# Kernel optimization log

Hardware: AMD Instinct MI355X
Metric: run time of the kernel (lower is better)

Reference implementation:

```python
import jax, jax.numpy as jnp
import numpy as np


def _temporal_gated_conv(x, W, b):
    """x: (B,T,N,C) -> (B,T-Kt+1,N,Co). W: (1,Kt,C,2*Co), b: (2*Co,).
    Matches torch Conv2d(in,2*out,(1,Kt)) over (B,C,N,T) followed by GLU."""
    xh = x.transpose(0, 2, 1, 3)  # (B,N,T,C) as NHWC, kernel (1,Kt) over (N,T)
    y = jax.lax.conv_general_dilated(
        xh, W, window_strides=(1, 1), padding='VALID',
        dimension_numbers=('NHWC', 'HWIO', 'NHWC')) + b  # (B,N,T',2Co)
    lhs, rhs = jnp.split(y, 2, axis=-1)
    y = lhs * jax.nn.sigmoid(rhs)
    return y.transpose(0, 2, 1, 3)  # (B,T',N,Co)


def _spatial_graph_conv(x, cheb, Theta):
    """x: (B,T,N,C), cheb: (K,N,N), Theta: (K,C,Co).
    Faithful to torch code: step_x is CUMULATIVELY multiplied by T_k."""
    K = cheb.shape[0]
    cur = x
    acc = jnp.zeros(x.shape[:3] + (Theta.shape[-1],), dtype=x.dtype)
    for k in range(K):  # K is small and structural
        cur = jnp.einsum('mn,btnc->btmc', cheb[k], cur)
        acc = acc + jnp.einsum('btnc,co->btno', cur, Theta[k])
    return jax.nn.relu(acc)


def setup_inputs() -> dict:
    key = jax.random.key(0)
    ks = jax.random.split(key, 7)
    B, T, N, C = 16, 64, 1024, 2
    Kt, Kc, temporal_dim, spatial_dim = 3, 3, 64, 16
    s = 0.05
    return {
        'x': jax.random.normal(ks[0], (B, T, N, C), jnp.float32),
        'cheb': jax.random.normal(ks[1], (Kc, N, N), jnp.float32) * (1.0 / np.sqrt(N)),
        'W1': jax.random.normal(ks[2], (1, Kt, C, 2 * temporal_dim), jnp.float32) * s,
        'b1': jax.random.normal(ks[3], (2 * temporal_dim,), jnp.float32) * s,
        'Theta': jax.random.normal(ks[4], (Kc, temporal_dim, spatial_dim), jnp.float32) * s,
        'W2': jax.random.normal(ks[5], (1, Kt, spatial_dim, 2 * temporal_dim), jnp.float32) * s,
        'b2': jax.random.normal(ks[6], (2 * temporal_dim,), jnp.float32) * s,
    }


def reference(x, cheb, W1, b1, Theta, W2, b2):
    h = _temporal_gated_conv(x, W1, b1)          # (B, T-Kt+1, N, temporal_dim)
    h = _spatial_graph_conv(h, cheb, Theta)      # (B, T-Kt+1, N, spatial_dim)
    out = _temporal_gated_conv(h, W2, b2)        # (B, T-2*(Kt-1), N, temporal_dim)
    return out
```

## Files before the change

### kernel.cpp

```cpp
#include <hip/hip_runtime.h>
#include <stdint.h>

typedef __attribute__((ext_vector_type(8))) short bf16x8;
typedef __attribute__((ext_vector_type(4))) float f32x4;

__device__ __forceinline__ unsigned short f2bf(float f) {
  union { float f; unsigned u; } v; v.f = f;
  unsigned r = v.u + 0x7FFFu + ((v.u >> 16) & 1u);
  return (unsigned short)(r >> 16);
}

__device__ __forceinline__ float sigm(float x) { return 1.0f / (1.0f + __expf(-x)); }

__device__ __forceinline__ void gload16(const void* g, void* l) {
  __builtin_amdgcn_global_load_lds((const __attribute__((address_space(1))) void*)g,
                                   (__attribute__((address_space(3))) void*)l, 16, 0, 0);
}

__device__ __forceinline__ void bar() {
  __builtin_amdgcn_sched_barrier(0);
  __builtin_amdgcn_s_barrier();
  __builtin_amdgcn_sched_barrier(0);
}

__global__ void k0t(const float* __restrict__ cheb, unsigned short* __restrict__ cb1,
                    unsigned short* __restrict__ cb2, unsigned short* __restrict__ Pbig,
                    unsigned short* __restrict__ t0, unsigned short* __restrict__ t1) {
  __shared__ unsigned short t[64][65];
  const int z = blockIdx.z;
  const int c = threadIdx.x & 63, r4 = threadIdx.x >> 6;
  const int r0 = blockIdx.y * 64, c0 = blockIdx.x * 64;
  const float* src = cheb + (size_t)z * 1048576;
#pragma unroll
  for (int r = 0; r < 64; r += 4) {
    const int rr = r0 + r + r4;
    const unsigned short h = f2bf(src[(size_t)rr * 1024 + c0 + c]);
    t[r + r4][c] = h;
    if (z == 0) Pbig[(size_t)rr * 3072 + c0 + c] = h;
    else if (z == 1) cb1[(size_t)rr * 1024 + c0 + c] = h;
    else cb2[(size_t)rr * 1024 + c0 + c] = h;
  }
  __syncthreads();
  if (z == 2) return;
  unsigned short* dst = z ? t1 : t0;
#pragma unroll
  for (int r = 0; r < 64; r += 4)
    dst[(size_t)(c0 + r + r4) * 1024 + r0 + c] = t[c][r + r4];
}

__global__ __launch_bounds__(256) void gemm_splitk(
    const unsigned short* __restrict__ A1, const unsigned short* __restrict__ B1,
    float* __restrict__ C1,
    const unsigned short* __restrict__ A2, const unsigned short* __restrict__ B2,
    float* __restrict__ C2) {
  __shared__ __align__(16) unsigned short sA[128 * 32];
  __shared__ __align__(16) unsigned short sB[128 * 32];
  const unsigned short* Ap = blockIdx.z ? A2 : A1;
  const unsigned short* Bp = blockIdx.z ? B2 : B1;
  float* Cp = blockIdx.z ? C2 : C1;
  const int mb = blockIdx.x & 7, nb = blockIdx.x >> 3, ks = blockIdx.y;
  const int tid = threadIdx.x;
  const int lane = tid & 63;
  const int w = tid >> 6;
  const int m0 = mb * 128, n0 = nb * 128;
  const int wm = (w >> 1) * 64, wn = (w & 1) * 64;
  const int lr = lane & 15, lg = lane >> 4;
  const f32x4 ZV = {0.f, 0.f, 0.f, 0.f};
  f32x4 acc[4][4];
#pragma unroll
  for (int f = 0; f < 4; ++f)
#pragma unroll
    for (int g = 0; g < 4; ++g) acc[f][g] = ZV;
  const int r2 = tid >> 2, kp = tid & 3;
  const size_t rowA0 = (size_t)(m0 + r2) * 1024;
  const size_t rowA1 = (size_t)(m0 + 64 + r2) * 1024;
  const size_t rowB0 = (size_t)(n0 + r2) * 1024;
  const size_t rowB1 = (size_t)(n0 + 64 + r2) * 1024;
  unsigned short* la = &sA[w * 512];
  unsigned short* lb = &sB[w * 512];
  const int kbase = ks * 256;
  for (int k0 = kbase; k0 < kbase + 256; k0 += 32) {
    const int kc = k0 + kp * 8;
    gload16(Ap + rowA0 + kc, la);
    gload16(Ap + rowA1 + kc, la + 2048);
    gload16(Bp + rowB0 + kc, lb);
    gload16(Bp + rowB1 + kc, lb + 2048);
    __syncthreads();
    bf16x8 av[4], bv[4];
#pragma unroll
    for (int f = 0; f < 4; ++f)
      av[f] = *(const bf16x8*)&sA[(wm + f * 16 + lr) * 32 + lg * 8];
#pragma unroll
    for (int g = 0; g < 4; ++g)
      bv[g] = *(const bf16x8*)&sB[(wn + g * 16 + lr) * 32 + lg * 8];
#pragma unroll
    for (int f = 0; f < 4; ++f)
#pragma unroll
      for (int g = 0; g < 4; ++g)
        acc[f][g] = __builtin_amdgcn_mfma_f32_16x16x32_bf16(av[f], bv[g], acc[f][g], 0, 0, 0);
    __syncthreads();
  }
  float* Cb = Cp + (size_t)ks * 1048576;
#pragma unroll
  for (int f = 0; f < 4; ++f) {
    const int m = m0 + wm + f * 16 + lg * 4;
#pragma unroll
    for (int g = 0; g < 4; ++g) {
      const int col = n0 + wn + g * 16 + lr;
#pragma unroll
      for (int i = 0; i < 4; ++i)
        Cb[(size_t)(m + i) * 1024 + col] = acc[f][g][i];
    }
  }
}

__global__ void reducep(const float* __restrict__ S1, unsigned short* __restrict__ D1, int ld1, int co1,
                        const float* __restrict__ S2, unsigned short* __restrict__ D2, int ld2, int co2) {
  const float* S = blockIdx.z ? S2 : S1;
  unsigned short* D = blockIdx.z ? D2 : D1;
  const int ld = blockIdx.z ? ld2 : ld1;
  const int co = blockIdx.z ? co2 : co1;
  const int e = (blockIdx.x * 256 + threadIdx.x) * 4;
  const float4 a = *(const float4*)&S[e];
  const float4 b = *(const float4*)&S[1048576 + e];
  const float4 c = *(const float4*)&S[2097152 + e];
  const float4 d = *(const float4*)&S[3145728 + e];
  const int row = e >> 10, col = e & 1023;
  ushort4 o;
  o.x = f2bf(a.x + b.x + c.x + d.x);
  o.y = f2bf(a.y + b.y + c.y + d.y);
  o.z = f2bf(a.z + b.z + c.z + d.z);
  o.w = f2bf(a.w + b.w + c.w + d.w);
  *(ushort4*)&D[(size_t)row * ld + co + col] = o;
}

__device__ __forceinline__ void dec_chunk(int s, int& row, int& c) {
  const int r3 = (((s >> 2) ^ (s >> 4)) & 1) | (((s >> 3) & 1) << 1) | (((s >> 4) & 1) << 2);
  const int u = s ^ r3;
  row = u >> 2;
  c = u & 3;
}

__global__ __launch_bounds__(512, 2) void gemm_big(
    const unsigned short* __restrict__ A, const unsigned short* __restrict__ Bt,
    unsigned short* __restrict__ C) {
  constexpr int K = 3072, NT = 96;
  __shared__ __align__(16) unsigned short lds[4 * 16384];
  const int tid = threadIdx.x;
  const int lane = tid & 63, w = tid >> 6;
  const int wr = w >> 2, wc = w & 3;
  const int lr = lane & 15, lg = lane >> 4;
  const int lin = blockIdx.x;
  const int v = (lin & 7) * 31 + (lin >> 3);
  const int mb = v & 3, nb = v >> 2;
  const int m0 = mb * 256, n0 = nb * 256;

  int r0_, c0_, r1_, c1_;
  dec_chunk((w * 2 + 0) * 64 + lane, r0_, c0_);
  dec_chunk((w * 2 + 1) * 64 + lane, r1_, c1_);
  const unsigned short* sA0 = A + (size_t)(m0 + r0_) * K + c0_ * 8;
  const unsigned short* sA1 = A + (size_t)(m0 + r1_) * K + c1_ * 8;
  const unsigned short* sB0 = Bt + (size_t)(n0 + r0_) * K + c0_ * 8;
  const unsigned short* sB1 = Bt + (size_t)(n0 + r1_) * K + c1_ * 8;
  const int ldsoff0 = (w * 2 + 0) * 512, ldsoff1 = (w * 2 + 1) * 512;

  f32x4 acc[8][4];
  const f32x4 ZV = {0.f, 0.f, 0.f, 0.f};
#pragma unroll
  for (int f = 0; f < 8; ++f)
#pragma unroll
    for (int g = 0; g < 4; ++g) acc[f][g] = ZV;

  const int aoff = (((wr * 128 + lr) * 64 + lg * 16) ^ ((lr & 7) << 4));
  const int boff = (((wc * 64 + lr) * 64 + lg * 16) ^ ((lr & 7) << 4));

  bf16x8 avA[8], bvA[4], avB[8], bvB[4];

#define STAGE(T)                                               \
  do {                                                         \
    unsigned short* ba_ = lds + ((T) & 3) * 16384;             \
    const int k0_ = (T) * 32;                                  \
    gload16(sA0 + k0_, ba_ + ldsoff0);                         \
    gload16(sA1 + k0_, ba_ + ldsoff1);                         \
    gload16(sB0 + k0_, ba_ + 8192 + ldsoff0);                  \
    gload16(sB1 + k0_, ba_ + 8192 + ldsoff1);                  \
  } while (0)

#define DSREAD(T, AN, BN)                                      \
  do {                                                         \
    const char* rb_ = (const char*)lds + ((T) & 3) * 32768;    \
    _Pragma("unroll") for (int f_ = 0; f_ < 8; ++f_)           \
      AN[f_] = *(const bf16x8*)(rb_ + aoff + f_ * 1024);       \
    _Pragma("unroll") for (int g_ = 0; g_ < 4; ++g_)           \
      BN[g_] = *(const bf16x8*)(rb_ + 16384 + boff + g_ * 1024); \
  } while (0)

#define MFMAC(AC, BC)                                          \
  do {                                                         \
    __builtin_amdgcn_s_setprio(1);                             \
    _Pragma("unroll") for (int f_ = 0; f_ < 8; ++f_)           \
      _Pragma("unroll") for (int g_ = 0; g_ < 4; ++g_)         \
        acc[f_][g_] = __builtin_amdgcn_mfma_f32_16x16x32_bf16(AC[f_], BC[g_], acc[f_][g_], 0, 0, 0); \
    __builtin_amdgcn_s_setprio(0);                             \
  } while (0)

  STAGE(0); STAGE(1); STAGE(2); STAGE(3);
  asm volatile("s_waitcnt vmcnt(8)" ::: "memory");
  bar();
  DSREAD(0, avA, bvA);

  for (int tt = 0; tt < NT - 4; tt += 2) {
    DSREAD(tt + 1, avB, bvB);
    STAGE(tt + 4);
    MFMAC(avA, bvA);
    asm volatile("s_waitcnt vmcnt(8) lgkmcnt(0)" ::: "memory");
    bar();
    DSREAD(tt + 2, avA, bvA);
    STAGE(tt + 5);
    MFMAC(avB, bvB);
    asm volatile("s_waitcnt vmcnt(8) lgkmcnt(0)" ::: "memory");
    bar();
  }
  DSREAD(93, avB, bvB);
  MFMAC(avA, bvA);
  asm volatile("s_waitcnt vmcnt(4) lgkmcnt(0)" ::: "memory");
  bar();
  DSREAD(94, avA, bvA);
  MFMAC(avB, bvB);
  asm volatile("s_waitcnt vmcnt(0) lgkmcnt(0)" ::: "memory");
  bar();
  DSREAD(95, avB, bvB);
  MFMAC(avA, bvA);
  asm volatile("s_waitcnt lgkmcnt(0)" ::: "memory");
  __builtin_amdgcn_sched_barrier(0);
  MFMAC(avB, bvB);
#undef STAGE
#undef DSREAD
#undef MFMAC

#pragma unroll
  for (int g = 0; g < 4; ++g) {
    const int n = n0 + wc * 64 + g * 16;
    const size_t jb = (size_t)(n >> 4) * 16384;
#pragma unroll
    for (int f = 0; f < 8; ++f) {
      const int m = m0 + wr * 128 + f * 16 + lg * 4;
#pragma unroll
      for (int i = 0; i < 4; ++i)
        C[jb + (size_t)(m + i) * 16 + lr] = f2bf(fmaxf(acc[f][g][i], 0.f));
    }
  }
}

__global__ __launch_bounds__(256) void k1_fused(
    const float* __restrict__ x, const float* __restrict__ W1, const float* __restrict__ b1,
    const float* __restrict__ Theta, unsigned short* __restrict__ Zt) {
  __shared__ __align__(16) unsigned short hs[4 * 64 * 68];
  __shared__ __align__(16) unsigned short th[3 * 16 * 72];
  __shared__ __align__(16) unsigned short tr[64 * 68];
  const int tid = threadIdx.x, lane = tid & 63, w = tid >> 6;
  const int n0 = blockIdx.x * 64;
  const int bt0 = blockIdx.y * 4;
  const int bt = bt0 + w;
  const int b = bt / 62, t = bt - b * 62;
  float xv[6];
#pragma unroll
  for (int kt = 0; kt < 3; ++kt) {
    const float2 p = *(const float2*)&x[(size_t)((b * 64 + t + kt) * 1024 + n0 + lane) * 2];
    xv[kt * 2] = p.x;
    xv[kt * 2 + 1] = p.y;
  }
  float h[64];
#pragma unroll
  for (int ch = 0; ch < 64; ++ch) {
    float l = b1[ch], r = b1[64 + ch];
#pragma unroll
    for (int q = 0; q < 6; ++q) {
      l += xv[q] * W1[q * 128 + ch];
      r += xv[q] * W1[q * 128 + 64 + ch];
    }
    h[ch] = l * sigm(r);
  }
#pragma unroll
  for (int c8 = 0; c8 < 8; ++c8) {
    union { unsigned short u[8]; uint4 v; } pk;
#pragma unroll
    for (int j = 0; j < 8; ++j) pk.u[j] = f2bf(h[c8 * 8 + j]);
    *(uint4*)&hs[(w * 64 + lane) * 68 + c8 * 8] = pk.v;
  }
  for (int idx = tid; idx < 3072; idx += 256) {
    const int kc = idx >> 10, o = (idx >> 6) & 15, c = idx & 63;
    th[kc * 1152 + o * 72 + c] = f2bf(Theta[((kc << 6) | c) * 16 + o]);
  }
  __syncthreads();
  const int lr = lane & 15, lg = lane >> 4;
  const f32x4 ZV = {0.f, 0.f, 0.f, 0.f};
  for (int kc = 0; kc < 3; ++kc) {
    const bf16x8 av0 = *(const bf16x8*)&th[kc * 1152 + lr * 72 + lg * 8];
    const bf16x8 av1 = *(const bf16x8*)&th[kc * 1152 + lr * 72 + 32 + lg * 8];
    f32x4 acc[4];
#pragma unroll
    for (int ns = 0; ns < 4; ++ns) acc[ns] = ZV;
#pragma unroll
    for (int ns = 0; ns < 4; ++ns) {
      const bf16x8 bv0 = *(const bf16x8*)&hs[(w * 64 + ns * 16 + lr) * 68 + lg * 8];
      const bf16x8 bv1 = *(const bf16x8*)&hs[(w * 64 + ns * 16 + lr) * 68 + 32 + lg * 8];
      acc[ns] = __builtin_amdgcn_mfma_f32_16x16x32_bf16(av0, bv0, acc[ns], 0, 0, 0);
      acc[ns] = __builtin_amdgcn_mfma_f32_16x16x32_bf16(av1, bv1, acc[ns], 0, 0, 0);
    }
    if (kc) __syncthreads();
#pragma unroll
    for (int ns = 0; ns < 4; ++ns)
#pragma unroll
      for (int i = 0; i < 4; ++i)
        tr[(w * 16 + lg * 4 + i) * 68 + ns * 16 + lr] = f2bf(acc[ns][i]);
    __syncthreads();
#pragma unroll
    for (int rd = 0; rd < 2; ++rd) {
      const int cidx = rd * 256 + tid;
      const int rl = cidx >> 3, ck = cidx & 7;
      const uint4 v = *(const uint4*)&tr[rl * 68 + ck * 8];
      *(uint4*)&Zt[(size_t)(bt0 * 16 + rl) * 3072 + kc * 1024 + n0 + ck * 8] = v;
    }
  }
}

__global__ __launch_bounds__(256) void k3_out(
    const unsigned short* __restrict__ accb, const float* __restrict__ W2,
    const float* __restrict__ b2, float* __restrict__ out) {
  __shared__ __align__(16) unsigned short sW[128 * 72];
  const int tid = threadIdx.x, lane = tid & 63, w = tid >> 6;
  const int lr = lane & 15, lg = lane >> 4;
  const int n0 = blockIdx.x * 256;
  const int btp = blockIdx.y;
  const int b = btp / 60, tt = btp - b * 60;
  for (int idx = tid; idx < 2048; idx += 256) {
    const int ch = idx >> 4, k = 48 + (idx & 15);
    sW[ch * 72 + k] = 0;
  }
  for (int idx = tid; idx < 6144; idx += 256) {
    const int k = idx >> 7, ch = idx & 127;
    sW[ch * 72 + k] = f2bf(W2[idx]);
  }
  const int rowb = n0 + w * 64;
  const bf16x8 ZB = {0, 0, 0, 0, 0, 0, 0, 0};
  bf16x8 av[4][2];
#pragma unroll
  for (int f = 0; f < 4; ++f)
#pragma unroll
    for (int hh = 0; hh < 2; ++hh) {
      const int gk = hh * 32 + lg * 8;
      const int kt = gk >> 4, ci = gk & 15;
      av[f][hh] = ZB;
      if (kt < 3)
        av[f][hh] = *(const bf16x8*)&accb[(size_t)(b * 62 + tt + kt) * 16384 +
                                          (size_t)(rowb + f * 16 + lr) * 16 + ci];
    }
  __syncthreads();
  const size_t obase = (size_t)(b * 60 + tt) * 65536;
  const f32x4 ZV = {0.f, 0.f, 0.f, 0.f};
#pragma unroll
  for (int gl = 0; gl < 4; ++gl) {
    const int chl = gl * 16 + lr;
    const bf16x8 bl0 = *(const bf16x8*)&sW[chl * 72 + lg * 8];
    const bf16x8 bl1 = *(const bf16x8*)&sW[chl * 72 + 32 + lg * 8];
    const bf16x8 br0 = *(const bf16x8*)&sW[(64 + chl) * 72 + lg * 8];
    const bf16x8 br1 = *(const bf16x8*)&sW[(64 + chl) * 72 + 32 + lg * 8];
    f32x4 aL[4], aR[4];
#pragma unroll
    for (int f = 0; f < 4; ++f) { aL[f] = ZV; aR[f] = ZV; }
#pragma unroll
    for (int f = 0; f < 4; ++f) {
      aL[f] = __builtin_amdgcn_mfma_f32_16x16x32_bf16(av[f][0], bl0, aL[f], 0, 0, 0);
      aL[f] = __builtin_amdgcn_mfma_f32_16x16x32_bf16(av[f][1], bl1, aL[f], 0, 0, 0);
      aR[f] = __builtin_amdgcn_mfma_f32_16x16x32_bf16(av[f][0], br0, aR[f], 0, 0, 0);
      aR[f] = __builtin_amdgcn_mfma_f32_16x16x32_bf16(av[f][1], br1, aR[f], 0, 0, 0);
    }
    const float bbl = b2[chl], bbr = b2[64 + chl];
#pragma unroll
    for (int f = 0; f < 4; ++f)
#pragma unroll
      for (int i = 0; i < 4; ++i) {
        const float pl = aL[f][i] + bbl;
        const float pr = aR[f][i] + bbr;
        out[obase + (size_t)(rowb + f * 16 + lg * 4 + i) * 64 + chl] = pl * sigm(pr);
      }
  }
}

extern "C" void kernel_launch(void* const* d_in, const int* in_sizes, int n_in,
                              void* d_out, int out_size, void* d_ws, size_t ws_size,
                              hipStream_t stream) {
  const float* x    = (const float*)d_in[0];
  const float* cheb = (const float*)d_in[1];
  const float* W1   = (const float*)d_in[2];
  const float* b1   = (const float*)d_in[3];
  const float* Th   = (const float*)d_in[4];
  const float* W2   = (const float*)d_in[5];
  const float* b2   = (const float*)d_in[6];
  float* out = (float*)d_out;

  char* ws = (char*)d_ws;
  const size_t MB = 1u << 20;
  unsigned short* cb1  = (unsigned short*)(ws);
  unsigned short* cb2  = (unsigned short*)(ws + 2 * MB);
  unsigned short* Pbig = (unsigned short*)(ws + 4 * MB);
  unsigned short* t0   = (unsigned short*)(ws + 10 * MB);
  unsigned short* t1   = (unsigned short*)(ws + 12 * MB);
  unsigned short* Qb   = (unsigned short*)(ws + 14 * MB);
  unsigned short* accb = (unsigned short*)(ws + 14 * MB);
  float*          P1f  = (float*)(ws + 48 * MB);
  float*          Qf   = (float*)(ws + 64 * MB);
  float*          P2f  = (float*)(ws + 80 * MB);
  unsigned short* Zt   = (unsigned short*)d_out;

  k0t<<<dim3(16, 16, 3), 256, 0, stream>>>(cheb, cb1, cb2, Pbig, t0, t1);
  gemm_splitk<<<dim3(64, 4, 2), 256, 0, stream>>>(cb1, t0, P1f, cb2, t1, Qf);
  reducep<<<dim3(1024, 1, 2), 256, 0, stream>>>(P1f, Pbig, 3072, 1024, Qf, Qb, 1024, 0);
  gemm_splitk<<<dim3(64, 4, 1), 256, 0, stream>>>(Qb, t0, P2f, Qb, t0, P2f);
  reducep<<<dim3(1024, 1, 1), 256, 0, stream>>>(P2f, Pbig, 3072, 2048, P2f, Pbig, 3072, 2048);
  k1_fused<<<dim3(16, 248), 256, 0, stream>>>(x, W1, b1, Th, Zt);
  gemm_big<<<dim3(248), dim3(512), 0, stream>>>(Pbig, Zt, accb);
  k3_out<<<dim3(4, 960), 256, 0, stream>>>(accb, W2, b2, out);
}
```

Before: 286.0 us.

## Restructure big GEMM main loop into split-phase ping-pong schedule with half-tile reads

Replaces the double-register-buffered main loop (8 A + 4 B fragments per stage, one MFMA burst per k-step) with a finer schedule that reads half of the A fragments at a time, splits the A and B global-to-LDS stages, and places barriers around each MFMA cluster. It uses fewer live fragment registers and interleaves LDS reads, global loads and MFMA bursts in the style of a ping-pong schedule. The aim is to overlap memory and compute more evenly across the two co-resident workgroups. The cost is many more barriers per k-step, which could stall the waves.

Result: slower. 291.9 us (+2.1%).

```diff
diff --git a/kernel.cpp b/kernel.cpp
--- a/kernel.cpp
+++ b/kernel.cpp
@@ -144,7 +144,7 @@
 __global__ __launch_bounds__(512, 2) void gemm_big(
     const unsigned short* __restrict__ A, const unsigned short* __restrict__ Bt,
     unsigned short* __restrict__ C) {
-  constexpr int K = 3072, NT = 96;
+  constexpr int K = 3072;
   __shared__ __align__(16) unsigned short lds[4 * 16384];
   const int tid = threadIdx.x;
   const int lane = tid & 63, w = tid >> 6;
@@ -174,69 +174,96 @@
   const int aoff = (((wr * 128 + lr) * 64 + lg * 16) ^ ((lr & 7) << 4));
   const int boff = (((wc * 64 + lr) * 64 + lg * 16) ^ ((lr & 7) << 4));
 
-  bf16x8 avA[8], bvA[4], avB[8], bvB[4];
-
-#define STAGE(T)                                               \
+  bf16x8 av[4], bv[4];
+
+#define STAGE_A(KS, BUF)                                       \
   do {                                                         \
-    unsigned short* ba_ = lds + ((T) & 3) * 16384;             \
-    const int k0_ = (T) * 32;                                  \
-    gload16(sA0 + k0_, ba_ + ldsoff0);                         \
-    gload16(sA1 + k0_, ba_ + ldsoff1);                         \
-    gload16(sB0 + k0_, ba_ + 8192 + ldsoff0);                  \
-    gload16(sB1 + k0_, ba_ + 8192 + ldsoff1);                  \
+    unsigned short* ba_ = lds + (BUF) * 16384;                 \
+    gload16(sA0 + (KS), ba_ + ldsoff0);                        \
+    gload16(sA1 + (KS), ba_ + ldsoff1);                        \
   } while (0)
-
-#define DSREAD(T, AN, BN)                                      \
+#define STAGE_B(KS, BUF)                                       \
   do {                                                         \
-    const char* rb_ = (const char*)lds + ((T) & 3) * 32768;    \
-    _Pragma("unroll") for (int f_ = 0; f_ < 8; ++f_)           \
-      AN[f_] = *(const bf16x8*)(rb_ + aoff + f_ * 1024);       \
-    _Pragma("unroll") for (int g_ = 0; g_ < 4; ++g_)           \
-      BN[g_] = *(const bf16x8*)(rb_ + 16384 + boff + g_ * 1024); \
+    unsigned short* ba_ = lds + (BUF) * 16384;                 \
+    gload16(sB0 + (KS), ba_ + 8192 + ldsoff0);                 \
+    gload16(sB1 + (KS), ba_ + 8192 + ldsoff1);                 \
   } while (0)
-
-#define MFMAC(AC, BC)                                          \
+#define RD_A(BUF, F0)                                          \
+  _Pragma("unroll") for (int f_ = 0; f_ < 4; ++f_)             \
+      av[f_] = *(const bf16x8*)((const char*)lds + (BUF) * 32768 + aoff + ((F0) + f_) * 1024);
+#define RD_B(BUF)                                              \
+  _Pragma("unroll") for (int g_ = 0; g_ < 4; ++g_)             \
+      bv[g_] = *(const bf16x8*)((const char*)lds + (BUF) * 32768 + 16384 + boff + g_ * 1024);
+#define MF(F0)                                                 \
   do {                                                         \
     __builtin_amdgcn_s_setprio(1);                             \
-    _Pragma("unroll") for (int f_ = 0; f_ < 8; ++f_)           \
+    _Pragma("unroll") for (int f_ = 0; f_ < 4; ++f_)           \
       _Pragma("unroll") for (int g_ = 0; g_ < 4; ++g_)         \
-        acc[f_][g_] = __builtin_amdgcn_mfma_f32_16x16x32_bf16(AC[f_], BC[g_], acc[f_][g_], 0, 0, 0); \
+        acc[(F0) + f_][g_] = __builtin_amdgcn_mfma_f32_16x16x32_bf16(av[f_], bv[g_], acc[(F0) + f_][g_], 0, 0, 0); \
     __builtin_amdgcn_s_setprio(0);                             \
   } while (0)
-
-  STAGE(0); STAGE(1); STAGE(2); STAGE(3);
-  asm volatile("s_waitcnt vmcnt(8)" ::: "memory");
-  bar();
-  DSREAD(0, avA, bvA);
-
-  for (int tt = 0; tt < NT - 4; tt += 2) {
-    DSREAD(tt + 1, avB, bvB);
-    STAGE(tt + 4);
-    MFMAC(avA, bvA);
-    asm volatile("s_waitcnt vmcnt(8) lgkmcnt(0)" ::: "memory");
-    bar();
-    DSREAD(tt + 2, avA, bvA);
-    STAGE(tt + 5);
-    MFMAC(avB, bvB);
-    asm volatile("s_waitcnt vmcnt(8) lgkmcnt(0)" ::: "memory");
-    bar();
-  }
-  DSREAD(93, avB, bvB);
-  MFMAC(avA, bvA);
-  asm volatile("s_waitcnt vmcnt(4) lgkmcnt(0)" ::: "memory");
-  bar();
-  DSREAD(94, avA, bvA);
-  MFMAC(avB, bvB);
-  asm volatile("s_waitcnt vmcnt(0) lgkmcnt(0)" ::: "memory");
-  bar();
-  DSREAD(95, avB, bvB);
-  MFMAC(avA, bvA);
-  asm volatile("s_waitcnt lgkmcnt(0)" ::: "memory");
+#define LG0                                                    \
+  asm volatile("s_waitcnt lgkmcnt(0)" ::: "memory");           \
   __builtin_amdgcn_sched_barrier(0);
-  MFMAC(avB, bvB);
-#undef STAGE
-#undef DSREAD
-#undef MFMAC
+#define VM8 asm volatile("s_waitcnt vmcnt(8)" ::: "memory");
+#define VM4 asm volatile("s_waitcnt vmcnt(4)" ::: "memory");
+#define VM0 asm volatile("s_waitcnt vmcnt(0)" ::: "memory");
+
+  STAGE_A(0, 0); STAGE_B(0, 0);
+  STAGE_A(32, 1); STAGE_B(32, 1);
+  STAGE_A(64, 2); STAGE_B(64, 2);
+  VM8; bar();
+
+#define TILE(TV, BE, BO, S1B, S2B)                             \
+  do {                                                         \
+    const int ks1_ = (2 * (TV) + 3) * 32;                      \
+    const int ks2_ = (2 * (TV) + 4) * 32;                      \
+    RD_A(BE, 0); RD_B(BE);                                     \
+    STAGE_A(ks1_, S1B);                                        \
+    bar(); LG0; MF(0); bar();                                  \
+    RD_A(BE, 4);                                               \
+    STAGE_B(ks1_, S1B);                                        \
+    bar(); LG0; MF(4); VM8; bar();                             \
+    RD_A(BO, 0); RD_B(BO);                                     \
+    STAGE_A(ks2_, S2B);                                        \
+    bar(); LG0; MF(0); bar();                                  \
+    RD_A(BO, 4);                                               \
+    STAGE_B(ks2_, S2B);                                        \
+    bar(); LG0; MF(4); VM8; bar();                             \
+  } while (0)
+
+  for (int T = 0; T < 46; T += 2) {
+    TILE(T, 0, 1, 3, 0);
+    TILE(T + 1, 2, 3, 1, 2);
+  }
+  RD_A(0, 0); RD_B(0);
+  STAGE_A(95 * 32, 3);
+  bar(); LG0; MF(0); bar();
+  RD_A(0, 4);
+  STAGE_B(95 * 32, 3);
+  bar(); LG0; MF(4); VM8; bar();
+  RD_A(1, 0); RD_B(1);
+  bar(); LG0; MF(0); bar();
+  RD_A(1, 4);
+  bar(); LG0; MF(4); VM4; bar();
+  RD_A(2, 0); RD_B(2);
+  bar(); LG0; MF(0); bar();
+  RD_A(2, 4);
+  bar(); LG0; MF(4); VM0; bar();
+  RD_A(3, 0); RD_B(3);
+  bar(); LG0; MF(0); bar();
+  RD_A(3, 4);
+  bar(); LG0; MF(4);
+#undef TILE
+#undef STAGE_A
+#undef STAGE_B
+#undef RD_A
+#undef RD_B
+#undef MF
+#undef LG0
+#undef VM8
+#undef VM4
+#undef VM0
 
 #pragma unroll
   for (int g = 0; g < 4; ++g) {
```

## Shrink gemm_big tile to 128x256 with triple-buffered LDS and 496 blocks

Applied to the files above, without the earlier changes.

Changes the big GEMM tile from 256x256 to 128x256, doubling the grid from 248 to 496 blocks. The LDS ring drops from four stages to three rotating slots, and launch bounds rise to allow four blocks per CU. The aim is better CU occupancy on a 256-CU part, where 248 blocks leave the GPU underfilled. In exchange each block does less reuse of the B tile (more global traffic per FLOP) and the pipeline is one stage shallower.

New measurement: 563.4 us. 96.9% more time.

```diff
diff --git a/kernel.cpp b/kernel.cpp
--- a/kernel.cpp
+++ b/kernel.cpp
@@ -141,95 +141,100 @@
   c = u & 3;
 }
 
-__global__ __launch_bounds__(512, 2) void gemm_big(
+__global__ __launch_bounds__(512, 4) void gemm_big(
     const unsigned short* __restrict__ A, const unsigned short* __restrict__ Bt,
     unsigned short* __restrict__ C) {
   constexpr int K = 3072, NT = 96;
-  __shared__ __align__(16) unsigned short lds[4 * 16384];
+  __shared__ __align__(16) unsigned short lds[3 * 12288];
   const int tid = threadIdx.x;
   const int lane = tid & 63, w = tid >> 6;
   const int wr = w >> 2, wc = w & 3;
   const int lr = lane & 15, lg = lane >> 4;
   const int lin = blockIdx.x;
-  const int v = (lin & 7) * 31 + (lin >> 3);
-  const int mb = v & 3, nb = v >> 2;
-  const int m0 = mb * 256, n0 = nb * 256;
-
-  int r0_, c0_, r1_, c1_;
-  dec_chunk((w * 2 + 0) * 64 + lane, r0_, c0_);
-  dec_chunk((w * 2 + 1) * 64 + lane, r1_, c1_);
-  const unsigned short* sA0 = A + (size_t)(m0 + r0_) * K + c0_ * 8;
-  const unsigned short* sA1 = A + (size_t)(m0 + r1_) * K + c1_ * 8;
-  const unsigned short* sB0 = Bt + (size_t)(n0 + r0_) * K + c0_ * 8;
-  const unsigned short* sB1 = Bt + (size_t)(n0 + r1_) * K + c1_ * 8;
-  const int ldsoff0 = (w * 2 + 0) * 512, ldsoff1 = (w * 2 + 1) * 512;
-
-  f32x4 acc[8][4];
+  const int v = (lin & 7) * 62 + (lin >> 3);
+  const int mb = v & 7, nb = v >> 3;
+  const int m0 = mb * 128, n0 = nb * 256;
+
+  int rA, cA, rB0, cB0, rB1, cB1;
+  dec_chunk(tid, rA, cA);
+  dec_chunk(tid, rB0, cB0);
+  dec_chunk(tid + 512, rB1, cB1);
+  const unsigned short* gA = A + (size_t)(m0 + rA) * K + cA * 8;
+  const unsigned short* gB0 = Bt + (size_t)(n0 + rB0) * K + cB0 * 8;
+  const unsigned short* gB1 = Bt + (size_t)(n0 + rB1) * K + cB1 * 8;
+  const int dA = tid * 8;
+  const int dB0 = 4096 + tid * 8;
+  const int dB1 = 4096 + tid * 8 + 4096;
+
+  f32x4 acc[4][4];
   const f32x4 ZV = {0.f, 0.f, 0.f, 0.f};
 #pragma unroll
-  for (int f = 0; f < 8; ++f)
+  for (int f = 0; f < 4; ++f)
 #pragma unroll
     for (int g = 0; g < 4; ++g) acc[f][g] = ZV;
 
-  const int aoff = (((wr * 128 + lr) * 64 + lg * 16) ^ ((lr & 7) << 4));
-  const int boff = (((wc * 64 + lr) * 64 + lg * 16) ^ ((lr & 7) << 4));
-
-  bf16x8 avA[8], bvA[4], avB[8], bvB[4];
-
-#define STAGE(T)                                               \
+  const int xo = ((lr * 64 + lg * 16) ^ ((lr & 7) << 4));
+  const int aoff = wr * 4096 + xo;
+  const int boff = 8192 + wc * 4096 + xo;
+
+  bf16x8 avA[4], bvA[4], avB[4], bvB[4];
+
+#define STAGE(T, SL)                                           \
   do {                                                         \
-    unsigned short* ba_ = lds + ((T) & 3) * 16384;             \
+    unsigned short* ba_ = lds + (SL) * 12288;                  \
     const int k0_ = (T) * 32;                                  \
-    gload16(sA0 + k0_, ba_ + ldsoff0);                         \
-    gload16(sA1 + k0_, ba_ + ldsoff1);                         \
-    gload16(sB0 + k0_, ba_ + 8192 + ldsoff0);                  \
-    gload16(sB1 + k0_, ba_ + 8192 + ldsoff1);                  \
+    gload16(gA + k0_, ba_ + dA);                               \
+    gload16(gB0 + k0_, ba_ + dB0);                             \
+    gload16(gB1 + k0_, ba_ + dB1);                             \
   } while (0)
 
-#define DSREAD(T, AN, BN)                                      \
+#define DSREAD(SL, AN, BN)                                     \
   do {                                                         \
-    const char* rb_ = (const char*)lds + ((T) & 3) * 32768;    \
-    _Pragma("unroll") for (int f_ = 0; f_ < 8; ++f_)           \
+    const char* rb_ = (const char*)lds + (SL) * 24576;         \
+    _Pragma("unroll") for (int f_ = 0; f_ < 4; ++f_)           \
       AN[f_] = *(const bf16x8*)(rb_ + aoff + f_ * 1024);       \
     _Pragma("unroll") for (int g_ = 0; g_ < 4; ++g_)           \
-      BN[g_] = *(const bf16x8*)(rb_ + 16384 + boff + g_ * 1024); \
+      BN[g_] = *(const bf16x8*)(rb_ + boff + g_ * 1024);       \
   } while (0)
 
 #define MFMAC(AC, BC)                                          \
   do {                                                         \
     __builtin_amdgcn_s_setprio(1);                             \
-    _Pragma("unroll") for (int f_ = 0; f_ < 8; ++f_)           \
+    _Pragma("unroll") for (int f_ = 0; f_ < 4; ++f_)           \
       _Pragma("unroll") for (int g_ = 0; g_ < 4; ++g_)         \
         acc[f_][g_] = __builtin_amdgcn_mfma_f32_16x16x32_bf16(AC[f_], BC[g_], acc[f_][g_], 0, 0, 0); \
     __builtin_amdgcn_s_setprio(0);                             \
   } while (0)
 
-  STAGE(0); STAGE(1); STAGE(2); STAGE(3);
-  asm volatile("s_waitcnt vmcnt(8)" ::: "memory");
+  STAGE(0, 0); STAGE(1, 1); STAGE(2, 2);
+  asm volatile("s_waitcnt vmcnt(3)" ::: "memory");
   bar();
   DSREAD(0, avA, bvA);
 
+  int sa = 0, sb = 1, sc = 2;
   for (int tt = 0; tt < NT - 4; tt += 2) {
-    DSREAD(tt + 1, avB, bvB);
-    STAGE(tt + 4);
+    DSREAD(sb, avB, bvB);
+    STAGE(tt + 3, sa);
     MFMAC(avA, bvA);
-    asm volatile("s_waitcnt vmcnt(8) lgkmcnt(0)" ::: "memory");
+    asm volatile("s_waitcnt vmcnt(3) lgkmcnt(0)" ::: "memory");
     bar();
-    DSREAD(tt + 2, avA, bvA);
-    STAGE(tt + 5);
+    DSREAD(sc, avA, bvA);
+    STAGE(tt + 4, sb);
     MFMAC(avB, bvB);
-    asm volatile("s_waitcnt vmcnt(8) lgkmcnt(0)" ::: "memory");
+    asm volatile("s_waitcnt vmcnt(3) lgkmcnt(0)" ::: "memory");
     bar();
-  }
-  DSREAD(93, avB, bvB);
+    const int t_ = sa; sa = sc; sc = sb; sb = t_;
+  }
+  DSREAD(0, avB, bvB);
+  STAGE(95, 2);
   MFMAC(avA, bvA);
-  asm volatile("s_waitcnt vmcnt(4) lgkmcnt(0)" ::: "memory");
+  asm volatile("s_waitcnt vmcnt(3) lgkmcnt(0)" ::: "memory");
   bar();
-  DSREAD(94, avA, bvA);
+  DSREAD(1, avA, bvA);
   MFMAC(avB, bvB);
   asm volatile("s_waitcnt vmcnt(0) lgkmcnt(0)" ::: "memory");
   bar();
-  DSREAD(95, avB, bvB);
+  DSREAD(2, avB, bvB);
   MFMAC(avA, bvA);
   asm volatile("s_waitcnt lgkmcnt(0)" ::: "memory");
   __builtin_amdgcn_sched_barrier(0);
@@ -243,8 +248,8 @@
     const int n = n0 + wc * 64 + g * 16;
     const size_t jb = (size_t)(n >> 4) * 16384;
 #pragma unroll
-    for (int f = 0; f < 8; ++f) {
-      const int m = m0 + wr * 128 + f * 16 + lg * 4;
+    for (int f = 0; f < 4; ++f) {
+      const int m = m0 + wr * 64 + f * 16 + lg * 4;
 #pragma unroll
       for (int i = 0; i < 4; ++i)
         C[jb + (size_t)(m + i) * 16 + lr] = f2bf(fmaxf(acc[f][g][i], 0.f));
@@ -420,6 +425,6 @@
   gemm_splitk<<<dim3(64, 4, 1), 256, 0, stream>>>(Qb, t0, P2f, Qb, t0, P2f);
   reducep<<<dim3(1024, 1, 1), 256, 0, stream>>>(P2f, Pbig, 3072, 2048, P2f, Pbig, 3072, 2048);
   k1_fused<<<dim3(16, 248), 256, 0, stream>>>(x, W1, b1, Th, Zt);
-  gemm_big<<<dim3(248), dim3(512), 0, stream>>>(Pbig, Zt, accb);
+  gemm_big<<<dim3(496), dim3(512), 0, stream>>>(Pbig, Zt, accb);
   k3_out<<<dim3(4, 960), 256, 0, stream>>>(accb, W2, b2, out);
 }
```
